# Kernel tuning notes

Hardware: AMD Instinct MI355X
Metric: run time of the kernel (lower is better)

## Reference

```python
import jax, jax.numpy as jnp
import numpy as np

B, D_IN, NF = 8192, 64, 128
D1 = 1 + D_IN              # 65  : first linear input (bias col + x)
O1 = 1 + NF                # 129 : o width after first layer
IN2 = O1 + NF * NF         # 16513 : polylayer-1 input width
O2 = O1 + NF               # 257
IN3 = O2 + NF * NF         # 16641 : polylayer-2 input width
FC_IN = 1 + 3 * NF + 3 * NF  # 769 : cat(o, og) width


def setup_inputs() -> dict:
    key = jax.random.key(0)
    ks = jax.random.split(key, 16)
    w = lambda k, shape: jax.random.normal(k, shape, jnp.float32) * 0.02
    return {
        "x": jax.random.normal(ks[0], (B, D_IN), jnp.float32),
        "bias0": jnp.asarray(1.0, jnp.float32),
        "Wf1": w(ks[1], (D1, NF)), "bf1": w(ks[2], (NF,)),
        "Wg1": w(ks[3], (D1, NF)), "bg1": w(ks[4], (NF,)),
        "Wf2": w(ks[5], (IN2, NF)), "bf2": w(ks[6], (NF,)),
        "Wg2": w(ks[7], (IN2, NF)), "bg2": w(ks[8], (NF,)),
        "Wf3": w(ks[9], (IN3, NF)), "bf3": w(ks[10], (NF,)),
        "Wg3": w(ks[11], (IN3, NF)), "bg3": w(ks[12], (NF,)),
        "Wfc": w(ks[13], (FC_IN, 1)), "bfc": w(ks[14], (1,)),
    }


def reference(x, bias0, Wf1, bf1, Wg1, bg1, Wf2, bf2, Wg2, bg2,
              Wf3, bf3, Wg3, bg3, Wfc, bfc):
    Bn = x.shape[0]
    o = jnp.ones((Bn, 1), x.dtype) * bias0          # bias column
    z = jnp.concatenate([o, x], axis=1)              # [B, 1+D_in]
    og = z @ Wg1 + bg1                               # vanishing branch
    ot = z @ Wf1 + bf1                               # nonvanishing branch
    o1 = ot                                          # degree-1 features, kept fixed
    o = jnp.concatenate([o, ot], axis=1)
    for Wf, bf, Wg, bg in ((Wf2, bf2, Wg2, bg2), (Wf3, bf3, Wg3, bg3)):
        # batched outer product o1_i ot_i^T, row-major flatten -> [B, nf1*nf_t]
        outer = (o1[:, :, None] * ot[:, None, :]).reshape(Bn, -1)
        xx = jnp.concatenate([o, outer], axis=1)
        xf = xx @ Wf + bf
        xg = xx @ Wg + bg
        ot = xf
        o = jnp.concatenate([o, xf], axis=1)
        og = jnp.concatenate([og, xg], axis=1)
    return jnp.concatenate([o, og], axis=1) @ Wfc + bfc
```

## Files before the change

### kernel.cpp

```cpp
#include <hip/hip_runtime.h>

typedef _Float16 f16;
typedef _Float16 f16x8 __attribute__((ext_vector_type(8)));
typedef float f32x4 __attribute__((ext_vector_type(4)));

static constexpr size_t PART_STRIDE = (size_t)8192 * 256;

static constexpr size_t OFF_W2   = 0;
static constexpr size_t SZ_W2    = (size_t)16512 * 256 * 2;
static constexpr size_t OFF_W3   = OFF_W2 + SZ_W2;
static constexpr size_t SZ_W3    = (size_t)16640 * 256 * 2;
static constexpr size_t OFF_OT1  = OFF_W3 + SZ_W3;
static constexpr size_t OFF_XF2  = OFF_OT1 + (size_t)8192 * 128 * 2;
static constexpr size_t OFF_C2   = OFF_XF2 + (size_t)8192 * 128 * 2;
static constexpr size_t OFF_C3   = OFF_C2 + 1024;
static constexpr size_t OFF_ACC  = OFF_C3 + 1024;
static constexpr size_t OFF_PART = OFF_ACC + 32768;

template<int LAYER>
__global__ __launch_bounds__(256)
void prep_w(const float* __restrict__ Wf, const float* __restrict__ Wg,
            f16* __restrict__ Wswz)
{
    const int t = blockIdx.x * 256 + threadIdx.x;
    const int s = t >> 10, rem = t & 1023;
    const int nt = rem >> 6, l = rem & 63;
    const int n = nt * 16 + (l & 15);
    const int kb = s * 32 + (l >> 4) * 8;
    f16x8 o;
#pragma unroll
    for (int e = 0; e < 8; ++e) {
        const int k = kb + e;
        int row;
        if (LAYER == 2) row = (k < 128) ? (1 + k) : (129 + (k - 128));
        else            row = (k < 128) ? (1 + k)
                              : ((k < 256) ? (129 + (k - 128)) : (257 + (k - 256)));
        const float v = (n < 128) ? Wf[(size_t)row * 128 + n]
                                  : Wg[(size_t)row * 128 + (n - 128)];
        o[e] = (f16)v;
    }
    *(f16x8*)(Wswz + (size_t)t * 8) = o;
}

__global__ __launch_bounds__(256)
void prep_small(const float* __restrict__ bias0,
                const float* __restrict__ Wf2, const float* __restrict__ bf2,
                const float* __restrict__ Wg2, const float* __restrict__ bg2,
                const float* __restrict__ Wf3, const float* __restrict__ bf3,
                const float* __restrict__ Wg3, const float* __restrict__ bg3,
                float* __restrict__ c2, float* __restrict__ c3)
{
    const int n = threadIdx.x;
    const float b0 = bias0[0];
    if (n < 128) { c2[n] = bf2[n] + b0 * Wf2[n]; c3[n] = bf3[n] + b0 * Wf3[n]; }
    else { const int m = n - 128; c2[n] = bg2[m] + b0 * Wg2[m]; c3[n] = bg3[m] + b0 * Wg3[m]; }
}

__global__ __launch_bounds__(256)
void layer1_poly(const float* __restrict__ x, const float* __restrict__ bias0,
                 const float* __restrict__ Wf1, const float* __restrict__ bf1,
                 const float* __restrict__ Wg1, const float* __restrict__ bg1,
                 const float* __restrict__ Wfc, const float* __restrict__ bfc,
                 f16* __restrict__ ot1f16, float* __restrict__ outacc)
{
    const int half = threadIdx.x >> 7;
    const int n = threadIdx.x & 127;
    const int r = blockIdx.x * 2 + half;
    const float b0 = bias0[0];
    float sf = b0 * Wf1[n] + bf1[n];
    float sg = b0 * Wg1[n] + bg1[n];
    const float* xr = x + (size_t)r * 64;
#pragma unroll 8
    for (int k = 0; k < 64; ++k) {
        const float xv = xr[k];
        sf = fmaf(xv, Wf1[(k + 1) * 128 + n], sf);
        sg = fmaf(xv, Wg1[(k + 1) * 128 + n], sg);
    }
    ot1f16[(size_t)r * 128 + (n ^ ((r & 7) << 3))] = (f16)sf;
    float p = sf * Wfc[1 + n] + sg * Wfc[385 + n];
#pragma unroll
    for (int off = 32; off; off >>= 1) p += __shfl_down(p, off);
    __shared__ float wp[4];
    if ((threadIdx.x & 63) == 0) wp[threadIdx.x >> 6] = p;
    __syncthreads();
    if ((threadIdx.x & 127) == 0)
        outacc[r] = bfc[0] + b0 * Wfc[0] + wp[half * 2] + wp[half * 2 + 1];
}

template<int LAYER>
__global__ __launch_bounds__(512)
void gemm_poly(const f16* __restrict__ Wswz, const f16* __restrict__ featg,
               const f16* __restrict__ ot1g, float* __restrict__ partials)
{
    extern __shared__ char smem[];
    f16* feat = (f16*)smem;
    f16* wbuf = (f16*)(smem + 32768);

    const int bid = blockIdx.x;
    const int rb = bid >> 2, sp = bid & 3;
    const int r0 = rb * 128;
    const int tid = threadIdx.x;

    for (int u = tid; u < 2048; u += 512)
        *(f16x8*)(feat + (size_t)u * 8) = *(const f16x8*)(featg + (size_t)r0 * 128 + (size_t)u * 8);

    const int NLIN = (LAYER == 2) ? 4 : 8;
    const int s_start = sp * 128 + (sp ? NLIN : 0);
    const int s_end = sp * 128 + 128 + NLIN;
    const int nst = s_end - s_start;

    const int wid = tid >> 6, lane = tid & 63;
    const int wr = wid >> 2, wc = wid & 3;
    const int lhi = lane >> 4, llo = lane & 15;

    f32x4 acc[4][4] = {};

    {
        const f16* src = Wswz + (size_t)s_start * 8192;
        *(f16x8*)(wbuf + tid * 16)     = *(const f16x8*)(src + tid * 16);
        *(f16x8*)(wbuf + tid * 16 + 8) = *(const f16x8*)(src + tid * 16 + 8);
    }
    __syncthreads();

    f16 o1h[4];
    int icur = -1;

    for (int c = 0; c < nst; ++c) {
        const int s = s_start + c;
        const bool more = (c + 1 < nst);
        f16x8 w0, w1;
        if (more) {
            const f16* src = Wswz + (size_t)(s + 1) * 8192;
            w0 = *(const f16x8*)(src + tid * 16);
            w1 = *(const f16x8*)(src + tid * 16 + 8);
        }

        f16x8 afr[4];
        if (s < NLIN) {
#pragma unroll
            for (int mi = 0; mi < 4; ++mi) {
                const int rl = wr * 64 + mi * 16 + llo;
                if (LAYER == 2) {
                    const int j0 = 32 * s + lhi * 8;
                    afr[mi] = *(const f16x8*)(feat + rl * 128 + (j0 ^ ((rl & 7) << 3)));
                } else if (s < 4) {
                    const int j0 = 32 * s + lhi * 8;
                    const int rg = r0 + rl;
                    afr[mi] = *(const f16x8*)(ot1g + (size_t)rg * 128 + (j0 ^ ((rg & 7) << 3)));
                } else {
                    const int j0 = 32 * (s - 4) + lhi * 8;
                    afr[mi] = *(const f16x8*)(feat + rl * 128 + (j0 ^ ((rl & 7) << 3)));
                }
            }
        } else {
            const int ku = (s - NLIN) * 32;
            const int i = ku >> 7;
            const int j0 = (ku & 127) + lhi * 8;
            if (i != icur) {
                icur = i;
#pragma unroll
                for (int mi = 0; mi < 4; ++mi) {
                    const int rl = wr * 64 + mi * 16 + llo;
                    if (LAYER == 2)
                        o1h[mi] = feat[rl * 128 + (i ^ ((rl & 7) << 3))];
                    else {
                        const int rg = r0 + rl;
                        o1h[mi] = ot1g[(size_t)rg * 128 + (i ^ ((rg & 7) << 3))];
                    }
                }
            }
#pragma unroll
            for (int mi = 0; mi < 4; ++mi) {
                const int rl = wr * 64 + mi * 16 + llo;
                const f16x8 sl = *(const f16x8*)(feat + rl * 128 + (j0 ^ ((rl & 7) << 3)));
                afr[mi] = sl * o1h[mi];
            }
        }

        const f16* wb = wbuf + (c & 1) * 8192;
#pragma unroll
        for (int ni = 0; ni < 4; ++ni) {
            const int nt = wc * 4 + ni;
            const f16x8 bfr = *(const f16x8*)(wb + (nt * 64 + lane) * 8);
#pragma unroll
            for (int mi = 0; mi < 4; ++mi)
                acc[mi][ni] = __builtin_amdgcn_mfma_f32_16x16x32_f16(afr[mi], bfr, acc[mi][ni], 0, 0, 0);
        }

        if (more) {
            f16* dst = wbuf + ((c + 1) & 1) * 8192;
            *(f16x8*)(dst + tid * 16)     = w0;
            *(f16x8*)(dst + tid * 16 + 8) = w1;
        }
        __syncthreads();
    }

    float* pout = partials + (size_t)sp * PART_STRIDE + (size_t)r0 * 256;
#pragma unroll
    for (int mi = 0; mi < 4; ++mi) {
#pragma unroll
        for (int ni = 0; ni < 4; ++ni) {
            const int col = wc * 64 + ni * 16 + llo;
            const int rbase = wr * 64 + mi * 16 + lhi * 4;
#pragma unroll
            for (int q = 0; q < 4; ++q)
                pout[(size_t)(rbase + q) * 256 + col] = acc[mi][ni][q];
        }
    }
}

template<int LAYER>
__global__ __launch_bounds__(256)
void reduce_poly(const float* __restrict__ partials, const float* __restrict__ cvec,
                 const float* __restrict__ Wfc, f16* __restrict__ xf_out,
                 float* __restrict__ outacc, float* __restrict__ outp)
{
    const int r = blockIdx.x;
    const int n = threadIdx.x;
    const size_t idx = (size_t)r * 256 + n;
    float v = partials[idx] + partials[idx + PART_STRIDE]
            + partials[idx + 2 * PART_STRIDE] + partials[idx + 3 * PART_STRIDE];
    v += cvec[n];
    if (LAYER == 2 && n < 128)
        xf_out[(size_t)r * 128 + (n ^ ((r & 7) << 3))] = (f16)v;
    const int wseg = (LAYER == 2) ? (n < 128 ? 129 + n : 513 + (n - 128))
                                  : (n < 128 ? 257 + n : 641 + (n - 128));
    float p = v * Wfc[wseg];
#pragma unroll
    for (int off = 32; off; off >>= 1) p += __shfl_down(p, off);
    __shared__ float wp[4];
    if ((threadIdx.x & 63) == 0) wp[threadIdx.x >> 6] = p;
    __syncthreads();
    if (threadIdx.x == 0) {
        const float tot = wp[0] + wp[1] + wp[2] + wp[3];
        if (LAYER == 2) outacc[r] += tot;
        else            outp[r] = outacc[r] + tot;
    }
}

extern "C" void kernel_launch(void* const* d_in, const int* in_sizes, int n_in,
                              void* d_out, int out_size, void* d_ws, size_t ws_size,
                              hipStream_t stream)
{
    (void)in_sizes; (void)n_in; (void)out_size; (void)ws_size;
    const float* x     = (const float*)d_in[0];
    const float* bias0 = (const float*)d_in[1];
    const float* Wf1   = (const float*)d_in[2];
    const float* bf1   = (const float*)d_in[3];
    const float* Wg1   = (const float*)d_in[4];
    const float* bg1   = (const float*)d_in[5];
    const float* Wf2   = (const float*)d_in[6];
    const float* bf2   = (const float*)d_in[7];
    const float* Wg2   = (const float*)d_in[8];
    const float* bg2   = (const float*)d_in[9];
    const float* Wf3   = (const float*)d_in[10];
    const float* bf3   = (const float*)d_in[11];
    const float* Wg3   = (const float*)d_in[12];
    const float* bg3   = (const float*)d_in[13];
    const float* Wfc   = (const float*)d_in[14];
    const float* bfc   = (const float*)d_in[15];
    float* out = (float*)d_out;

    char* ws = (char*)d_ws;
    f16*   W2s    = (f16*)(ws + OFF_W2);
    f16*   W3s    = (f16*)(ws + OFF_W3);
    f16*   ot1f16 = (f16*)(ws + OFF_OT1);
    f16*   xf2f16 = (f16*)(ws + OFF_XF2);
    float* c2     = (float*)(ws + OFF_C2);
    float* c3     = (float*)(ws + OFF_C3);
    float* outacc = (float*)(ws + OFF_ACC);
    float* parts  = (float*)(ws + OFF_PART);

    prep_w<2><<<2064, 256, 0, stream>>>(Wf2, Wg2, W2s);
    prep_w<3><<<2080, 256, 0, stream>>>(Wf3, Wg3, W3s);
    prep_small<<<1, 256, 0, stream>>>(bias0, Wf2, bf2, Wg2, bg2, Wf3, bf3, Wg3, bg3, c2, c3);
    layer1_poly<<<4096, 256, 0, stream>>>(x, bias0, Wf1, bf1, Wg1, bg1, Wfc, bfc, ot1f16, outacc);
    gemm_poly<2><<<256, 512, 65536, stream>>>(W2s, ot1f16, ot1f16, parts);
    reduce_poly<2><<<8192, 256, 0, stream>>>(parts, c2, Wfc, xf2f16, outacc, out);
    gemm_poly<3><<<256, 512, 65536, stream>>>(W3s, xf2f16, ot1f16, parts);
    reduce_poly<3><<<8192, 256, 0, stream>>>(parts, c3, Wfc, nullptr, outacc, out);
}
```

Before: 359.9 us.

## Restructure poly GEMM: K-split by outer-product column, register-resident features, async LDS weight loads

```diff
diff --git a/kernel.cpp b/kernel.cpp
--- a/kernel.cpp
+++ b/kernel.cpp
@@ -7,9 +7,9 @@
 static constexpr size_t PART_STRIDE = (size_t)8192 * 256;
 
 static constexpr size_t OFF_W2   = 0;
-static constexpr size_t SZ_W2    = (size_t)16512 * 256 * 2;
+static constexpr size_t SZ_W2    = (size_t)516 * 8192 * 2;
 static constexpr size_t OFF_W3   = OFF_W2 + SZ_W2;
-static constexpr size_t SZ_W3    = (size_t)16640 * 256 * 2;
+static constexpr size_t SZ_W3    = (size_t)520 * 8192 * 2;
 static constexpr size_t OFF_OT1  = OFF_W3 + SZ_W3;
 static constexpr size_t OFF_XF2  = OFF_OT1 + (size_t)8192 * 128 * 2;
 static constexpr size_t OFF_C2   = OFF_XF2 + (size_t)8192 * 128 * 2;
@@ -26,15 +26,19 @@
     const int s = t >> 10, rem = t & 1023;
     const int nt = rem >> 6, l = rem & 63;
     const int n = nt * 16 + (l & 15);
-    const int kb = s * 32 + (l >> 4) * 8;
+    const int klb = (l >> 4) * 8;
     f16x8 o;
 #pragma unroll
     for (int e = 0; e < 8; ++e) {
-        const int k = kb + e;
+        const int kl = klb + e;
         int row;
-        if (LAYER == 2) row = (k < 128) ? (1 + k) : (129 + (k - 128));
-        else            row = (k < 128) ? (1 + k)
-                              : ((k < 256) ? (129 + (k - 128)) : (257 + (k - 256)));
+        if (LAYER == 2) {
+            if (s < 4) row = 1 + s * 32 + kl;
+            else { const int u = s - 4; row = 129 + (u & 127) * 128 + (u >> 7) * 32 + kl; }
+        } else {
+            if (s < 8) row = 1 + s * 32 + kl;
+            else { const int u = s - 8; row = 257 + (u & 127) * 128 + (u >> 7) * 32 + kl; }
+        }
         const float v = (n < 128) ? Wf[(size_t)row * 128 + n]
                                   : Wg[(size_t)row * 128 + (n - 128)];
         o[e] = (f16)v;
@@ -76,7 +80,7 @@
         sf = fmaf(xv, Wf1[(k + 1) * 128 + n], sf);
         sg = fmaf(xv, Wg1[(k + 1) * 128 + n], sg);
     }
-    ot1f16[(size_t)r * 128 + (n ^ ((r & 7) << 3))] = (f16)sf;
+    ot1f16[(size_t)r * 128 + n] = (f16)sf;
     float p = sf * Wfc[1 + n] + sg * Wfc[385 + n];
 #pragma unroll
     for (int off = 32; off; off >>= 1) p += __shfl_down(p, off);
@@ -87,127 +91,121 @@
         outacc[r] = bfc[0] + b0 * Wfc[0] + wp[half * 2] + wp[half * 2 + 1];
 }
 
+
+#define STAGE(S_W, BUF) do {                                                        \
+    const f16* _src = wsrc0 + (size_t)(S_W) * 8192;                                 \
+    __builtin_amdgcn_global_load_lds(                                               \
+        (const __attribute__((address_space(1))) unsigned int*)_src,                \
+        (__attribute__((address_space(3))) unsigned int*)&wbuf[BUF][tid * 8],       \
+        16, 0, 0);                                                                  \
+} while (0)
+
+#define GBODY(O1CUR, O1NXT, I8)                                                     \
+{                                                                                   \
+    _Pragma("unroll")                                                               \
+    for (int e = 0; e < 8; ++e) {                                                   \
+        const int cc = (I8) * 8 + e;                                                \
+        if (e < 7) { STAGE(out_base + cc + 1, (CLIN + e + 1) & 1); }                \
+        else if ((I8) < 15) { STAGE(out_base + cc + 1, (CLIN + e + 1) & 1); }       \
+        if (e == 0) {                                                               \
+            _Pragma("unroll")                                                       \
+            for (int mi = 0; mi < 8; ++mi)                                          \
+                O1NXT[mi] = *(const f16x8*)(ot1_row + mi * 2048 + ((I8) + 1) * 8);  \
+        }                                                                           \
+        f16x8 afr[8];                                                               \
+        _Pragma("unroll")                                                           \
+        for (int mi = 0; mi < 8; ++mi)                                              \
+            afr[mi] = featreg[mi] * O1CUR[mi][e];                                   \
+        const f16* wb = &wbuf[(CLIN + e) & 1][0];                                   \
+        _Pragma("unroll")                                                           \
+        for (int ni = 0; ni < 2; ++ni) {                                            \
+            const f16x8 bfr = *(const f16x8*)(wb + ((wc * 2 + ni) * 64 + lane) * 8);\
+            _Pragma("unroll")                                                       \
+            for (int mi = 0; mi < 8; ++mi)                                          \
+                acc[mi][ni] = __builtin_amdgcn_mfma_f32_16x16x32_f16(               \
+                    afr[mi], bfr, acc[mi][ni], 0, 0, 0);                            \
+        }                                                                           \
+        __syncthreads();                                                            \
+    }                                                                               \
+}
+
 template<int LAYER>
-__global__ __launch_bounds__(512)
-void gemm_poly(const f16* __restrict__ Wswz, const f16* __restrict__ featg,
-               const f16* __restrict__ ot1g, float* __restrict__ partials)
-{
-    extern __shared__ char smem[];
-    f16* feat = (f16*)smem;
-    f16* wbuf = (f16*)(smem + 32768);
+__global__ __launch_bounds__(256, 2)
+void gemm_poly(const f16* __restrict__ Wswz, const f16* featg,
+               const f16* ot1g, float* __restrict__ partials)
+{
+    __shared__ f16 wbuf[2][2048];
+
+    constexpr int NLIN = (LAYER == 2) ? 4 : 8;
+    constexpr int CLIN = (LAYER == 2) ? 1 : 2;
 
     const int bid = blockIdx.x;
-    const int rb = bid >> 2, sp = bid & 3;
-    const int r0 = rb * 128;
+    const int rb = bid >> 4;
+    const int sp = (bid >> 2) & 3;
+    const int nb = bid & 3;
+    const int r0 = rb * 256;
     const int tid = threadIdx.x;
-
-    for (int u = tid; u < 2048; u += 512)
-        *(f16x8*)(feat + (size_t)u * 8) = *(const f16x8*)(featg + (size_t)r0 * 128 + (size_t)u * 8);
-
-    const int NLIN = (LAYER == 2) ? 4 : 8;
-    const int s_start = sp * 128 + (sp ? NLIN : 0);
-    const int s_end = sp * 128 + 128 + NLIN;
-    const int nst = s_end - s_start;
-
     const int wid = tid >> 6, lane = tid & 63;
-    const int wr = wid >> 2, wc = wid & 3;
+    const int wr = wid >> 1, wc = wid & 1;
     const int lhi = lane >> 4, llo = lane & 15;
 
-    f32x4 acc[4][4] = {};
-
-    {
-        const f16* src = Wswz + (size_t)s_start * 8192;
-        *(f16x8*)(wbuf + tid * 16)     = *(const f16x8*)(src + tid * 16);
-        *(f16x8*)(wbuf + tid * 16 + 8) = *(const f16x8*)(src + tid * 16 + 8);
+    const f16* wsrc0 = Wswz + nb * 2048 + tid * 8;
+    const f16* ot1_row  = ot1g  + (size_t)(r0 + wr * 128 + llo) * 128;
+    const f16* feat_row = featg + (size_t)(r0 + wr * 128 + llo) * 128;
+
+    f32x4 acc[8][2] = {};
+    const int out_base = NLIN + sp * 128;
+
+    STAGE(CLIN * sp, 0);
+    f16x8 featreg[8], o1A[8], o1B[8];
+#pragma unroll
+    for (int mi = 0; mi < 8; ++mi) {
+        featreg[mi] = *(const f16x8*)(feat_row + mi * 2048 + sp * 32 + lhi * 8);
+        o1A[mi]     = *(const f16x8*)(ot1_row + mi * 2048);
     }
     __syncthreads();
 
-    f16 o1h[4];
-    int icur = -1;
-
-    for (int c = 0; c < nst; ++c) {
-        const int s = s_start + c;
-        const bool more = (c + 1 < nst);
-        f16x8 w0, w1;
-        if (more) {
-            const f16* src = Wswz + (size_t)(s + 1) * 8192;
-            w0 = *(const f16x8*)(src + tid * 16);
-            w1 = *(const f16x8*)(src + tid * 16 + 8);
+#pragma unroll
+    for (int c = 0; c < CLIN; ++c) {
+        const int s = CLIN * sp + c;
+        STAGE((c + 1 < CLIN) ? (s + 1) : out_base, (c + 1) & 1);
+        f16x8 afr[8];
+        const int col = s * 32 + lhi * 8;
+#pragma unroll
+        for (int mi = 0; mi < 8; ++mi) {
+            if (LAYER == 2) afr[mi] = *(const f16x8*)(ot1_row + mi * 2048 + col);
+            else afr[mi] = (col < 128) ? *(const f16x8*)(ot1_row + mi * 2048 + col)
+                                       : *(const f16x8*)(feat_row + mi * 2048 + (col - 128));
         }
-
-        f16x8 afr[4];
-        if (s < NLIN) {
-#pragma unroll
-            for (int mi = 0; mi < 4; ++mi) {
-                const int rl = wr * 64 + mi * 16 + llo;
-                if (LAYER == 2) {
-                    const int j0 = 32 * s + lhi * 8;
-                    afr[mi] = *(const f16x8*)(feat + rl * 128 + (j0 ^ ((rl & 7) << 3)));
-                } else if (s < 4) {
-                    const int j0 = 32 * s + lhi * 8;
-                    const int rg = r0 + rl;
-                    afr[mi] = *(const f16x8*)(ot1g + (size_t)rg * 128 + (j0 ^ ((rg & 7) << 3)));
-                } else {
-                    const int j0 = 32 * (s - 4) + lhi * 8;
-                    afr[mi] = *(const f16x8*)(feat + rl * 128 + (j0 ^ ((rl & 7) << 3)));
-                }
-            }
-        } else {
-            const int ku = (s - NLIN) * 32;
-            const int i = ku >> 7;
-            const int j0 = (ku & 127) + lhi * 8;
-            if (i != icur) {
-                icur = i;
-#pragma unroll
-                for (int mi = 0; mi < 4; ++mi) {
-                    const int rl = wr * 64 + mi * 16 + llo;
-                    if (LAYER == 2)
-                        o1h[mi] = feat[rl * 128 + (i ^ ((rl & 7) << 3))];
-                    else {
-                        const int rg = r0 + rl;
-                        o1h[mi] = ot1g[(size_t)rg * 128 + (i ^ ((rg & 7) << 3))];
-                    }
-                }
-            }
-#pragma unroll
-            for (int mi = 0; mi < 4; ++mi) {
-                const int rl = wr * 64 + mi * 16 + llo;
-                const f16x8 sl = *(const f16x8*)(feat + rl * 128 + (j0 ^ ((rl & 7) << 3)));
-                afr[mi] = sl * o1h[mi];
-            }
-        }
-
-        const f16* wb = wbuf + (c & 1) * 8192;
-#pragma unroll
-        for (int ni = 0; ni < 4; ++ni) {
-            const int nt = wc * 4 + ni;
-            const f16x8 bfr = *(const f16x8*)(wb + (nt * 64 + lane) * 8);
-#pragma unroll
-            for (int mi = 0; mi < 4; ++mi)
+        const f16* wb = &wbuf[c & 1][0];
+#pragma unroll
+        for (int ni = 0; ni < 2; ++ni) {
+            const f16x8 bfr = *(const f16x8*)(wb + ((wc * 2 + ni) * 64 + lane) * 8);
+#pragma unroll
+            for (int mi = 0; mi < 8; ++mi)
                 acc[mi][ni] = __builtin_amdgcn_mfma_f32_16x16x32_f16(afr[mi], bfr, acc[mi][ni], 0, 0, 0);
         }
-
-        if (more) {
-            f16* dst = wbuf + ((c + 1) & 1) * 8192;
-            *(f16x8*)(dst + tid * 16)     = w0;
-            *(f16x8*)(dst + tid * 16 + 8) = w1;
-        }
         __syncthreads();
     }
 
-    float* pout = partials + (size_t)sp * PART_STRIDE + (size_t)r0 * 256;
-#pragma unroll
-    for (int mi = 0; mi < 4; ++mi) {
-#pragma unroll
-        for (int ni = 0; ni < 4; ++ni) {
-            const int col = wc * 64 + ni * 16 + llo;
-            const int rbase = wr * 64 + mi * 16 + lhi * 4;
+    for (int i8 = 0; i8 < 16; i8 += 2) {
+        GBODY(o1A, o1B, i8);
+        GBODY(o1B, o1A, i8 + 1);
+    }
+
+    float* pout = partials + (size_t)sp * PART_STRIDE
+                + (size_t)(r0 + wr * 128) * 256 + nb * 64 + wc * 32 + llo;
+#pragma unroll
+    for (int mi = 0; mi < 8; ++mi)
+#pragma unroll
+        for (int ni = 0; ni < 2; ++ni)
 #pragma unroll
             for (int q = 0; q < 4; ++q)
-                pout[(size_t)(rbase + q) * 256 + col] = acc[mi][ni][q];
-        }
-    }
-}
+                pout[(size_t)(mi * 16 + lhi * 4 + q) * 256 + ni * 16] = acc[mi][ni][q];
+}
+
+#undef GBODY
+#undef STAGE
 
 template<int LAYER>
 __global__ __launch_bounds__(256)
@@ -222,7 +220,7 @@
             + partials[idx + 2 * PART_STRIDE] + partials[idx + 3 * PART_STRIDE];
     v += cvec[n];
     if (LAYER == 2 && n < 128)
-        xf_out[(size_t)r * 128 + (n ^ ((r & 7) << 3))] = (f16)v;
+        xf_out[(size_t)r * 128 + n] = (f16)v;
     const int wseg = (LAYER == 2) ? (n < 128 ? 129 + n : 513 + (n - 128))
                                   : (n < 128 ? 257 + n : 641 + (n - 128));
     float p = v * Wfc[wseg];
@@ -275,8 +273,8 @@
     prep_w<3><<<2080, 256, 0, stream>>>(Wf3, Wg3, W3s);
     prep_small<<<1, 256, 0, stream>>>(bias0, Wf2, bf2, Wg2, bg2, Wf3, bf3, Wg3, bg3, c2, c3);
     layer1_poly<<<4096, 256, 0, stream>>>(x, bias0, Wf1, bf1, Wg1, bg1, Wfc, bfc, ot1f16, outacc);
-    gemm_poly<2><<<256, 512, 65536, stream>>>(W2s, ot1f16, ot1f16, parts);
+    gemm_poly<2><<<512, 256, 0, stream>>>(W2s, ot1f16, ot1f16, parts);
     reduce_poly<2><<<8192, 256, 0, stream>>>(parts, c2, Wfc, xf2f16, outacc, out);
-    gemm_poly<3><<<256, 512, 65536, stream>>>(W3s, xf2f16, ot1f16, parts);
+    gemm_poly<3><<<512, 256, 0, stream>>>(W3s, xf2f16, ot1f16, parts);
     reduce_poly<3><<<8192, 256, 0, stream>>>(parts, c3, Wfc, nullptr, outacc, out);
 }
```

After: 312.6 us. 1.15x faster.
